# Kernel tuning notes

Hardware: AMD Instinct MI355X
Metric: run time of the kernel (lower is better)

Reference implementation:

```python
import jax, jax.numpy as jnp
import numpy as np

N_HEADS = 4
DIM_HEAD = 32


def setup_inputs() -> dict:
    key = jax.random.key(0)
    k1, k2, k3, k4 = jax.random.split(key, 4)
    x = jax.random.normal(k1, (8, 64, 80, 1024), dtype=jnp.float32)
    # conv_qkv: 1x1 conv, no bias -> weight [3*heads*dim_head, dim_in_out]
    w_qkv = jax.random.normal(k2, (3 * N_HEADS * DIM_HEAD, 64), dtype=jnp.float32) * 0.05
    # conv_out: 1x1 conv with bias -> weight [dim_in_out, heads*dim_head], bias [dim_in_out]
    w_out = jax.random.normal(k3, (64, N_HEADS * DIM_HEAD), dtype=jnp.float32) * 0.05
    b_out = jax.random.normal(k4, (64,), dtype=jnp.float32) * 0.05
    return {"x": x, "w_qkv": w_qkv, "w_out": w_out, "b_out": b_out}


def reference(x, w_qkv, w_out, b_out):
    b, c, h, w = x.shape
    n = h * w
    # 1x1 conv == channel matmul
    qkv = jnp.einsum('bchw,oc->bohw', x, w_qkv)            # [b, 3*heads*dh, h, w]
    qkv = qkv.reshape(b, 3, N_HEADS, DIM_HEAD, n)          # qkv outermost, then heads, then c
    q, k, v = qkv[:, 0], qkv[:, 1], qkv[:, 2]              # each [b, heads, dh, n]
    k = jax.nn.softmax(k, axis=-1)                          # softmax over spatial positions
    context = jnp.einsum('bhdn,bhen->bhde', k, v)          # [b, heads, dh, dh]
    out = jnp.einsum('bhde,bhdn->bhen', context, q)        # [b, heads, dh, n]
    out = out.reshape(b, N_HEADS * DIM_HEAD, h, w)
    return jnp.einsum('bchw,oc->bohw', out, w_out) + b_out[None, :, None, None]
```

## Files before the change

kernel.cpp:

```cpp
#include <hip/hip_runtime.h>
#include <stdint.h>


#define N_POS 81920
#define NT    128
#define TILES 640

typedef short bf16x8 __attribute__((ext_vector_type(8)));
typedef float f32x4  __attribute__((ext_vector_type(4)));

__device__ __forceinline__ uint32_t packbf(float lo, float hi){
  uint32_t a = __float_as_uint(lo), b = __float_as_uint(hi);
  a = (a + 0x8000u) >> 16;
  b = (b + 0x8000u) & 0xffff0000u;
  return a | b;
}
__device__ __forceinline__ short bf16of(float v){
  return (short)((__float_as_uint(v) + 0x8000u) >> 16);
}

__global__ __launch_bounds__(512, 4) void kernA(
    const float* __restrict__ x, const float* __restrict__ w,
    float* __restrict__ pA, float* __restrict__ pZ, int nch, int tpc)
{
  __shared__ __align__(16) uint16_t xs_cp[64 * 136];
  __shared__ __align__(16) uint16_t xs_pc[128 * 72];
  __shared__ __align__(16) uint16_t es[128 * 136];

  const int t  = threadIdx.x;
  const int w8 = t >> 6;
  const int l  = t & 63;
  const int lm = l & 15;
  const int lg = l >> 4;

  const int b  = blockIdx.x / nch;
  const int ch = blockIdx.x % nch;
  const float* xb = x + (size_t)b * 64 * N_POS;

  const int rr  = t >> 3;
  const int pg  = t & 7;
  const int spp = t & 127;
  const int scg = t >> 7;

  const int pth = w8 & 3;
  const int ht0 = (w8 >> 2) * 4;

  bf16x8 wkf[4][2];
  #pragma unroll
  for (int i = 0; i < 4; ++i)
    #pragma unroll
    for (int kk = 0; kk < 2; ++kk){
      const float* wp = w + (size_t)(128 + 16*(ht0+i) + lm) * 64 + 32*kk + 8*lg;
      float4 w0 = *(const float4*)wp;
      float4 w1 = *(const float4*)(wp + 4);
      bf16x8 f;
      f[0]=bf16of(w0.x); f[1]=bf16of(w0.y); f[2]=bf16of(w0.z); f[3]=bf16of(w0.w);
      f[4]=bf16of(w1.x); f[5]=bf16of(w1.y); f[6]=bf16of(w1.z); f[7]=bf16of(w1.w);
      wkf[i][kk] = f;
    }

  bf16x8 ones;
  #pragma unroll
  for (int j = 0; j < 8; ++j) ones[j] = (short)0x3F80;

  f32x4 acc[4], zac;
  zac = (f32x4){0.f,0.f,0.f,0.f};
  #pragma unroll
  for (int n = 0; n < 4; ++n) acc[n] = (f32x4){0.f,0.f,0.f,0.f};

  float4 fa0, fa1, fa2, fa3;
  float v[16];
  {
    const int n0 = (ch * tpc) * NT;
    const float* ga = xb + (size_t)rr * N_POS + n0 + 16*pg;
    fa0 = *(const float4*)ga;       fa1 = *(const float4*)(ga + 4);
    fa2 = *(const float4*)(ga + 8); fa3 = *(const float4*)(ga + 12);
    const float* gb = xb + (size_t)(16*scg) * N_POS + n0 + spp;
    #pragma unroll
    for (int i = 0; i < 16; ++i) v[i] = gb[(size_t)i * N_POS];
  }

  for (int tile = 0; tile < tpc; ++tile){
    __syncthreads();
    {
      uint4 u0, u1;
      u0.x = packbf(fa0.x,fa0.y); u0.y = packbf(fa0.z,fa0.w);
      u0.z = packbf(fa1.x,fa1.y); u0.w = packbf(fa1.z,fa1.w);
      u1.x = packbf(fa2.x,fa2.y); u1.y = packbf(fa2.z,fa2.w);
      u1.z = packbf(fa3.x,fa3.y); u1.w = packbf(fa3.z,fa3.w);
      *(uint4*)&xs_cp[rr*136 + 16*pg]     = u0;
      *(uint4*)&xs_cp[rr*136 + 16*pg + 8] = u1;
      uint4 p0, p1;
      p0.x = packbf(v[0],v[1]);   p0.y = packbf(v[2],v[3]);
      p0.z = packbf(v[4],v[5]);   p0.w = packbf(v[6],v[7]);
      p1.x = packbf(v[8],v[9]);   p1.y = packbf(v[10],v[11]);
      p1.z = packbf(v[12],v[13]); p1.w = packbf(v[14],v[15]);
      *(uint4*)&xs_pc[spp*72 + 16*scg]     = p0;
      *(uint4*)&xs_pc[spp*72 + 16*scg + 8] = p1;
    }
    __syncthreads();
    if (tile + 1 < tpc){
      const int n1 = (ch * tpc + tile + 1) * NT;
      const float* ga = xb + (size_t)rr * N_POS + n1 + 16*pg;
      fa0 = *(const float4*)ga;       fa1 = *(const float4*)(ga + 4);
      fa2 = *(const float4*)(ga + 8); fa3 = *(const float4*)(ga + 12);
      const float* gb = xb + (size_t)(16*scg) * N_POS + n1 + spp;
      #pragma unroll
      for (int i = 0; i < 16; ++i) v[i] = gb[(size_t)i * N_POS];
    }
    #pragma unroll
    for (int ip = 0; ip < 2; ++ip){
      const int pt = pth + 4*ip;
      bf16x8 af0 = *(const bf16x8*)&xs_pc[(16*pt + lm)*72 + 8*lg];
      bf16x8 af1 = *(const bf16x8*)&xs_pc[(16*pt + lm)*72 + 32 + 8*lg];
      #pragma unroll
      for (int i = 0; i < 4; ++i){
        f32x4 s = (f32x4){0.f,0.f,0.f,0.f};
        s = __builtin_amdgcn_mfma_f32_16x16x32_bf16(af0, wkf[i][0], s, 0,0,0);
        s = __builtin_amdgcn_mfma_f32_16x16x32_bf16(af1, wkf[i][1], s, 0,0,0);
        float e0 = __expf(s[0]), e1 = __expf(s[1]);
        float e2 = __expf(s[2]), e3 = __expf(s[3]);
        uint2 pk; pk.x = packbf(e0,e1); pk.y = packbf(e2,e3);
        *(uint2*)&es[(16*(ht0+i) + lm)*136 + 16*pt + 4*lg] = pk;
      }
    }
    __syncthreads();
    __builtin_amdgcn_s_setprio(1);
    #pragma unroll
    for (int kk = 0; kk < 4; ++kk){
      bf16x8 ea = *(const bf16x8*)&es[(16*w8 + lm)*136 + 32*kk + 8*lg];
      bf16x8 xbf[4];
      #pragma unroll
      for (int n = 0; n < 4; ++n)
        xbf[n] = *(const bf16x8*)&xs_cp[(16*n + lm)*136 + 32*kk + 8*lg];
      #pragma unroll
      for (int n = 0; n < 4; ++n)
        acc[n] = __builtin_amdgcn_mfma_f32_16x16x32_bf16(ea, xbf[n], acc[n], 0,0,0);
      zac = __builtin_amdgcn_mfma_f32_16x16x32_bf16(ea, ones, zac, 0,0,0);
    }
    __builtin_amdgcn_s_setprio(0);
  }

  float* pa = pA + (size_t)blockIdx.x * 8192;
  const int hd0 = 16*w8 + 4*lg;
  #pragma unroll
  for (int n = 0; n < 4; ++n)
    #pragma unroll
    for (int r = 0; r < 4; ++r)
      pa[(size_t)(hd0 + r)*64 + 16*n + lm] = acc[n][r];
  if (lm == 0){
    #pragma unroll
    for (int r = 0; r < 4; ++r)
      pZ[(size_t)blockIdx.x * 128 + hd0 + r] = zac[r];
  }
}

__global__ __launch_bounds__(256) void kernR1(
    const float* __restrict__ pA, const float* __restrict__ pZ,
    float* __restrict__ Ar, float* __restrict__ Zr, int nch)
{
  const int b = blockIdx.x >> 3, s = blockIdx.x & 7;
  const int off = s * 1024 + threadIdx.x * 4;
  float4 a = make_float4(0.f, 0.f, 0.f, 0.f);
  for (int ch = 0; ch < nch; ++ch){
    float4 v = *(const float4*)&pA[(size_t)(b * nch + ch) * 8192 + off];
    a.x += v.x; a.y += v.y; a.z += v.z; a.w += v.w;
  }
  *(float4*)&Ar[(size_t)b * 8192 + off] = a;
  if (s == 0 && threadIdx.x < 128){
    float z = 0.f;
    for (int ch = 0; ch < nch; ++ch) z += pZ[(size_t)(b * nch + ch) * 128 + threadIdx.x];
    Zr[b * 128 + threadIdx.x] = z;
  }
}

__global__ __launch_bounds__(256) void kernCM(
    const float* __restrict__ Ar, const float* __restrict__ Zr,
    const float* __restrict__ w_qkv, const float* __restrict__ w_out,
    float* __restrict__ M)
{
  __shared__ float A[128 * 65];
  __shared__ float Z[128];
  __shared__ float cs[128 * 33];
  __shared__ float T[64 * 129];
  const int b = blockIdx.x, t = threadIdx.x;

  #pragma unroll
  for (int k = 0; k < 32; ++k){
    int i = t + 256 * k;
    A[(i >> 6) * 65 + (i & 63)] = Ar[(size_t)b * 8192 + i];
  }
  if (t < 128) Z[t] = Zr[b * 128 + t];
  __syncthreads();

  {
    const int hd = t & 127, h = hd >> 5, e0 = (t >> 7) * 16;
    const float rz = 1.0f / Z[hd];
    for (int je = 0; je < 16; ++je){
      int e = e0 + je;
      const float* wv = w_qkv + (size_t)(256 + 32 * h + e) * 64;
      float a = 0.f;
      #pragma unroll
      for (int c = 0; c < 64; ++c) a = fmaf(A[hd * 65 + c], wv[c], a);
      cs[hd * 33 + e] = a * rz;
    }
  }
  __syncthreads();

  const int o = t & 63, g = t >> 6;
  for (int jh = 0; jh < 32; ++jh){
    int hd = 32 * g + jh;
    const float* wo = w_out + (size_t)o * 128 + 32 * g;
    float a = 0.f;
    #pragma unroll
    for (int e = 0; e < 32; ++e) a = fmaf(wo[e], cs[hd * 33 + e], a);
    T[o * 129 + hd] = a;
  }
  __syncthreads();

  const int c0 = 16 * g;
  float m[16];
  #pragma unroll
  for (int j = 0; j < 16; ++j) m[j] = 0.f;
  for (int hd = 0; hd < 128; ++hd){
    float tv = T[o * 129 + hd];
    const float* wq = w_qkv + (size_t)hd * 64 + c0;
    #pragma unroll
    for (int j = 0; j < 16; ++j) m[j] = fmaf(tv, wq[j], m[j]);
  }
  #pragma unroll
  for (int j = 0; j < 16; ++j) M[(size_t)b * 4096 + o * 64 + c0 + j] = m[j];
}

__global__ __launch_bounds__(256, 2) void kernO(
    const float* __restrict__ x, const float* __restrict__ M,
    const float* __restrict__ b_out, float* __restrict__ out)
{
  __shared__ __align__(16) uint16_t xs[2][256 * 72];

  const int t  = threadIdx.x;
  const int wv = t >> 6;
  const int l  = t & 63;
  const int lm = l & 15;
  const int lg = l >> 4;

  const int b  = blockIdx.x >> 6;
  const int tg = blockIdx.x & 63;
  const float* xb = x   + (size_t)b * 64 * N_POS + tg * 1280;
  float*       ob = out + (size_t)b * 64 * N_POS + tg * 1280;

  const float* Mb = M + (size_t)b * 4096;
  bf16x8 mb[4][2];
  float bias[4];
  #pragma unroll
  for (int ot = 0; ot < 4; ++ot){
    bias[ot] = b_out[16*ot + lm];
    #pragma unroll
    for (int kk = 0; kk < 2; ++kk){
      const float* mp = Mb + (size_t)(16*ot + lm)*64 + 32*kk + 8*lg;
      float4 m0 = *(const float4*)mp;
      float4 m1 = *(const float4*)(mp + 4);
      bf16x8 f;
      f[0]=bf16of(m0.x); f[1]=bf16of(m0.y); f[2]=bf16of(m0.z); f[3]=bf16of(m0.w);
      f[4]=bf16of(m1.x); f[5]=bf16of(m1.y); f[6]=bf16of(m1.z); f[7]=bf16of(m1.w);
      mb[ot][kk] = f;
    }
  }

  uint4 st[8];

  #pragma unroll
  for (int cc = 0; cc < 8; ++cc){
    float v[8];
    #pragma unroll
    for (int j = 0; j < 8; ++j)
      v[j] = xb[(size_t)(8*cc + j) * N_POS + t];
    st[cc].x = packbf(v[0],v[1]); st[cc].y = packbf(v[2],v[3]);
    st[cc].z = packbf(v[4],v[5]); st[cc].w = packbf(v[6],v[7]);
  }
  #pragma unroll
  for (int cc = 0; cc < 8; ++cc)
    *(uint4*)&xs[0][t*72 + 8*cc] = st[cc];
  __syncthreads();

  for (int tile = 0; tile < 5; ++tile){
    const int cur = tile & 1;
    if (tile < 4){
      const float* gn = xb + (tile + 1) * 256 + t;
      #pragma unroll
      for (int cc = 0; cc < 8; ++cc){
        float v[8];
        #pragma unroll
        for (int j = 0; j < 8; ++j)
          v[j] = gn[(size_t)(8*cc + j) * N_POS];
        st[cc].x = packbf(v[0],v[1]); st[cc].y = packbf(v[2],v[3]);
        st[cc].z = packbf(v[4],v[5]); st[cc].w = packbf(v[6],v[7]);
      }
    }
    const int pp0 = tile * 256;
    #pragma unroll
    for (int ip = 0; ip < 4; ++ip){
      const int pt = 4*wv + ip;
      bf16x8 af0 = *(const bf16x8*)&xs[cur][(16*pt + lm)*72 + 8*lg];
      bf16x8 af1 = *(const bf16x8*)&xs[cur][(16*pt + lm)*72 + 32 + 8*lg];
      #pragma unroll
      for (int ot = 0; ot < 4; ++ot){
        f32x4 d = (f32x4){0.f,0.f,0.f,0.f};
        d = __builtin_amdgcn_mfma_f32_16x16x32_bf16(af0, mb[ot][0], d, 0,0,0);
        d = __builtin_amdgcn_mfma_f32_16x16x32_bf16(af1, mb[ot][1], d, 0,0,0);
        float4 stv = make_float4(d[0]+bias[ot], d[1]+bias[ot],
                                 d[2]+bias[ot], d[3]+bias[ot]);
        *(float4*)&ob[(size_t)(16*ot + lm) * N_POS + pp0 + 16*pt + 4*lg] = stv;
      }
    }
    if (tile < 4){
      #pragma unroll
      for (int cc = 0; cc < 8; ++cc)
        *(uint4*)&xs[cur ^ 1][t*72 + 8*cc] = st[cc];
      __syncthreads();
    }
  }
}

extern "C" void kernel_launch(void* const* d_in, const int* in_sizes, int n_in,
                              void* d_out, int out_size, void* d_ws, size_t ws_size,
                              hipStream_t stream)
{
  const float* x     = (const float*)d_in[0];
  const float* w_qkv = (const float*)d_in[1];
  const float* w_out = (const float*)d_in[2];
  const float* b_out = (const float*)d_in[3];
  float* out = (float*)d_out;
  float* ws  = (float*)d_ws;

  static const int cand[] = {64, 40, 32, 20, 16, 10, 8, 5, 4, 2, 1};
  int nch = 1;
  for (int i = 0; i < 11; ++i){
    size_t need = ((size_t)8 * cand[i] * (8192 + 128)
                   + 8 * 8192 + 8 * 128 + (size_t)8 * 4096) * 4;
    if (need <= ws_size){ nch = cand[i]; break; }
  }
  const int tpc = TILES / nch;

  float* pA  = ws;
  float* pZ  = pA + (size_t)8 * nch * 8192;
  float* Ar  = pZ + (size_t)8 * nch * 128;
  float* Zr  = Ar + (size_t)8 * 8192;
  float* M   = Zr + (size_t)8 * 128;

  kernA<<<8 * nch, 512, 0, stream>>>(x, w_qkv, pA, pZ, nch, tpc);
  kernR1<<<64,     256, 0, stream>>>(pA, pZ, Ar, Zr, nch);
  kernCM<<<8,      256, 0, stream>>>(Ar, Zr, w_qkv, w_out, M);
  kernO<<<512,     256, 0, stream>>>(x, M, b_out, out);
}
```

Measured before the change: 209.4 us.

## Cache bf16 position-major copy of x in kernA and read it in kernO

kernA now writes its shared-memory bf16 position-major tile of x out to a workspace buffer with nontemporal stores. The output kernel reads this half-size, already transposed copy directly into MFMA fragments, with no LDS staging and no fp32 re-read of x. The grid grows to 2560 blocks and occupancy rises. This trades an extra 84MB of writes in kernA for halving kernO's input reads, and it needs a large workspace; otherwise it falls back to the old path.

```diff
diff --git a/kernel.cpp b/kernel.cpp
--- a/kernel.cpp
+++ b/kernel.cpp
@@ -8,6 +8,7 @@
 
 typedef short bf16x8 __attribute__((ext_vector_type(8)));
 typedef float f32x4  __attribute__((ext_vector_type(4)));
+typedef uint32_t u32x4 __attribute__((ext_vector_type(4)));
 
 __device__ __forceinline__ uint32_t packbf(float lo, float hi){
   uint32_t a = __float_as_uint(lo), b = __float_as_uint(hi);
@@ -21,7 +22,8 @@
 
 __global__ __launch_bounds__(512, 4) void kernA(
     const float* __restrict__ x, const float* __restrict__ w,
-    float* __restrict__ pA, float* __restrict__ pZ, int nch, int tpc)
+    float* __restrict__ pA, float* __restrict__ pZ,
+    uint16_t* __restrict__ x16, int nch, int tpc)
 {
   __shared__ __align__(16) uint16_t xs_cp[64 * 136];
   __shared__ __align__(16) uint16_t xs_pc[128 * 72];
@@ -81,6 +83,7 @@
   }
 
   for (int tile = 0; tile < tpc; ++tile){
+    const int n0 = (ch * tpc + tile) * NT;
     __syncthreads();
     {
       uint4 u0, u1;
@@ -100,13 +103,21 @@
     }
     __syncthreads();
     if (tile + 1 < tpc){
-      const int n1 = (ch * tpc + tile + 1) * NT;
+      const int n1 = n0 + NT;
       const float* ga = xb + (size_t)rr * N_POS + n1 + 16*pg;
       fa0 = *(const float4*)ga;       fa1 = *(const float4*)(ga + 4);
       fa2 = *(const float4*)(ga + 8); fa3 = *(const float4*)(ga + 12);
       const float* gb = xb + (size_t)(16*scg) * N_POS + n1 + spp;
       #pragma unroll
       for (int i = 0; i < 16; ++i) v[i] = gb[(size_t)i * N_POS];
+    }
+    if (x16){
+      const int pos = t >> 2, q = t & 3;
+      u32x4 q0 = *(const u32x4*)&xs_pc[pos*72 + 16*q];
+      u32x4 q1 = *(const u32x4*)&xs_pc[pos*72 + 16*q + 8];
+      uint16_t* dst = x16 + ((size_t)b * N_POS + n0 + pos) * 64 + 16*q;
+      __builtin_nontemporal_store(q0, (u32x4*)&dst[0]);
+      __builtin_nontemporal_store(q1, (u32x4*)&dst[8]);
     }
     #pragma unroll
     for (int ip = 0; ip < 2; ++ip){
@@ -232,22 +243,19 @@
   for (int j = 0; j < 16; ++j) M[(size_t)b * 4096 + o * 64 + c0 + j] = m[j];
 }
 
-__global__ __launch_bounds__(256, 2) void kernO(
-    const float* __restrict__ x, const float* __restrict__ M,
+__global__ __launch_bounds__(256, 4) void kernO(
+    const uint16_t* __restrict__ x16, const float* __restrict__ M,
     const float* __restrict__ b_out, float* __restrict__ out)
 {
-  __shared__ __align__(16) uint16_t xs[2][256 * 72];
-
   const int t  = threadIdx.x;
   const int wv = t >> 6;
   const int l  = t & 63;
   const int lm = l & 15;
   const int lg = l >> 4;
 
-  const int b  = blockIdx.x >> 6;
-  const int tg = blockIdx.x & 63;
-  const float* xb = x   + (size_t)b * 64 * N_POS + tg * 1280;
-  float*       ob = out + (size_t)b * 64 * N_POS + tg * 1280;
+  const int b  = blockIdx.x / 320;
+  const int p0 = (blockIdx.x % 320) * 256;
+  const uint16_t* xb = x16 + ((size_t)b * N_POS + p0) * 64;
 
   const float* Mb = M + (size_t)b * 4096;
   bf16x8 mb[4][2];
@@ -267,8 +275,67 @@
     }
   }
 
+  bf16x8 af0[4], af1[4];
+  #pragma unroll
+  for (int ip = 0; ip < 4; ++ip){
+    const int row = 16*(4*wv + ip) + lm;
+    af0[ip] = *(const bf16x8*)&xb[row*64 + 8*lg];
+    af1[ip] = *(const bf16x8*)&xb[row*64 + 32 + 8*lg];
+  }
+
+  float* ob = out + (size_t)b * 64 * N_POS + p0;
+
+  #pragma unroll
+  for (int ip = 0; ip < 4; ++ip){
+    const int pt = 4*wv + ip;
+    #pragma unroll
+    for (int ot = 0; ot < 4; ++ot){
+      f32x4 d = (f32x4){0.f,0.f,0.f,0.f};
+      d = __builtin_amdgcn_mfma_f32_16x16x32_bf16(af0[ip], mb[ot][0], d, 0,0,0);
+      d = __builtin_amdgcn_mfma_f32_16x16x32_bf16(af1[ip], mb[ot][1], d, 0,0,0);
+      float4 st = make_float4(d[0]+bias[ot], d[1]+bias[ot],
+                              d[2]+bias[ot], d[3]+bias[ot]);
+      *(float4*)&ob[(size_t)(16*ot + lm) * N_POS + 16*pt + 4*lg] = st;
+    }
+  }
+}
+
+__global__ __launch_bounds__(256, 2) void kernO_f32(
+    const float* __restrict__ x, const float* __restrict__ M,
+    const float* __restrict__ b_out, float* __restrict__ out)
+{
+  __shared__ __align__(16) uint16_t xs[2][256 * 72];
+
+  const int t  = threadIdx.x;
+  const int wv = t >> 6;
+  const int l  = t & 63;
+  const int lm = l & 15;
+  const int lg = l >> 4;
+
+  const int b  = blockIdx.x >> 6;
+  const int tg = blockIdx.x & 63;
+  const float* xb = x   + (size_t)b * 64 * N_POS + tg * 1280;
+  float*       ob = out + (size_t)b * 64 * N_POS + tg * 1280;
+
+  const float* Mb = M + (size_t)b * 4096;
+  bf16x8 mb[4][2];
+  float bias[4];
+  #pragma unroll
+  for (int ot = 0; ot < 4; ++ot){
+    bias[ot] = b_out[16*ot + lm];
+    #pragma unroll
+    for (int kk = 0; kk < 2; ++kk){
+      const float* mp = Mb + (size_t)(16*ot + lm)*64 + 32*kk + 8*lg;
+      float4 m0 = *(const float4*)mp;
+      float4 m1 = *(const float4*)(mp + 4);
+      bf16x8 f;
+      f[0]=bf16of(m0.x); f[1]=bf16of(m0.y); f[2]=bf16of(m0.z); f[3]=bf16of(m0.w);
+      f[4]=bf16of(m1.x); f[5]=bf16of(m1.y); f[6]=bf16of(m1.z); f[7]=bf16of(m1.w);
+      mb[ot][kk] = f;
+    }
+  }
+
   uint4 st[8];
-
   #pragma unroll
   for (int cc = 0; cc < 8; ++cc){
     float v[8];
@@ -333,23 +400,42 @@
   float* out = (float*)d_out;
   float* ws  = (float*)d_ws;
 
-  static const int cand[] = {64, 40, 32, 20, 16, 10, 8, 5, 4, 2, 1};
-  int nch = 1;
-  for (int i = 0; i < 11; ++i){
-    size_t need = ((size_t)8 * cand[i] * (8192 + 128)
-                   + 8 * 8192 + 8 * 128 + (size_t)8 * 4096) * 4;
-    if (need <= ws_size){ nch = cand[i]; break; }
-  }
-  const int tpc = TILES / nch;
-
-  float* pA  = ws;
-  float* pZ  = pA + (size_t)8 * nch * 8192;
-  float* Ar  = pZ + (size_t)8 * nch * 128;
-  float* Zr  = Ar + (size_t)8 * 8192;
-  float* M   = Zr + (size_t)8 * 128;
-
-  kernA<<<8 * nch, 512, 0, stream>>>(x, w_qkv, pA, pZ, nch, tpc);
-  kernR1<<<64,     256, 0, stream>>>(pA, pZ, Ar, Zr, nch);
-  kernCM<<<8,      256, 0, stream>>>(Ar, Zr, w_qkv, w_out, M);
-  kernO<<<512,     256, 0, stream>>>(x, M, b_out, out);
-}
+  const size_t x16_bytes = (size_t)8 * N_POS * 64 * 2;
+  const size_t fixed     = ((size_t)8*8192 + 8*128 + 8*4096) * 4;
+  const size_t part64    = (size_t)8 * 64 * (8192 + 128) * 4;
+
+  const bool use16 = (x16_bytes + fixed + part64) <= ws_size;
+
+  if (use16){
+    const int nch = 64, tpc = TILES / 64;
+    uint16_t* x16 = (uint16_t*)ws;
+    float* pA  = (float*)(ws + x16_bytes / 4);
+    float* pZ  = pA + (size_t)8 * nch * 8192;
+    float* Ar  = pZ + (size_t)8 * nch * 128;
+    float* Zr  = Ar + (size_t)8 * 8192;
+    float* M   = Zr + (size_t)8 * 128;
+
+    kernA<<<8 * nch, 512, 0, stream>>>(x, w_qkv, pA, pZ, x16, nch, tpc);
+    kernR1<<<64,     256, 0, stream>>>(pA, pZ, Ar, Zr, nch);
+    kernCM<<<8,      256, 0, stream>>>(Ar, Zr, w_qkv, w_out, M);
+    kernO<<<2560,    256, 0, stream>>>(x16, M, b_out, out);
+  } else {
+    static const int cand[] = {64, 40, 32, 20, 16, 10, 8, 5, 4, 2, 1};
+    int nch = 1;
+    for (int i = 0; i < 11; ++i){
+      size_t need = ((size_t)8 * cand[i] * (8192 + 128)) * 4 + fixed;
+      if (need <= ws_size){ nch = cand[i]; break; }
+    }
+    const int tpc = TILES / nch;
+    float* pA  = ws;
+    float* pZ  = pA + (size_t)8 * nch * 8192;
+    float* Ar  = pZ + (size_t)8 * nch * 128;
+    float* Zr  = Ar + (size_t)8 * 8192;
+    float* M   = Zr + (size_t)8 * 128;
+
+    kernA<<<8 * nch, 512, 0, stream>>>(x, w_qkv, pA, pZ, nullptr, nch, tpc);
+    kernR1<<<64,     256, 0, stream>>>(pA, pZ, Ar, Zr, nch);
+    kernCM<<<8,      256, 0, stream>>>(Ar, Zr, w_qkv, w_out, M);
+    kernO_f32<<<512, 256, 0, stream>>>(x, M, b_out, out);
+  }
+}
```

Result: slower. 226.6 us (+8.2%).
